# Performance work log

Measured on AMD Instinct MI355X. Metric: run time of the kernel, lower is better.

The kernel has to match this reference:

```python
import jax, jax.numpy as jnp
import numpy as np

HEADS = 16
DIM_HEAD = 128
SCALE = DIM_HEAD ** -0.5


def rotate_half(x):
    # x: (..., d) with d even; pairs (x1, x2) -> (-x2, x1)
    x = x.reshape(*x.shape[:-1], -1, 2)
    x1, x2 = x[..., 0], x[..., 1]
    return jnp.stack([-x2, x1], axis=-1).reshape(*x.shape[:-2], -1)


def apply_rotary(freqs, t):
    # freqs: (n, d), t: (b, h, n, d)
    cos = jnp.cos(freqs)[None, None]
    sin = jnp.sin(freqs)[None, None]
    return t * cos + rotate_half(t) * sin


def setup_inputs() -> dict:
    key = jax.random.key(0)
    ks = jax.random.split(key, 6)
    b, n, dim = 2, 2048, 2048
    inner = HEADS * DIM_HEAD
    s = dim ** -0.5
    x = jax.random.normal(ks[0], (b, n, dim), dtype=jnp.float32)
    rotary_emb = jax.random.normal(ks[1], (n, DIM_HEAD), dtype=jnp.float32)
    Wq = jax.random.normal(ks[2], (dim, inner), dtype=jnp.float32) * s
    Wkv = jax.random.normal(ks[3], (dim, 2 * inner), dtype=jnp.float32) * s
    Wo = jax.random.normal(ks[4], (inner, dim), dtype=jnp.float32) * s
    bo = jnp.zeros((dim,), dtype=jnp.float32)
    return {"x": x, "rotary_emb": rotary_emb, "Wq": Wq, "Wkv": Wkv, "Wo": Wo, "bo": bo}


def reference(x, rotary_emb, Wq, Wkv, Wo, bo):
    b, n, _ = x.shape
    q = x @ Wq                      # (b, n, inner)
    kv = x @ Wkv                    # (b, n, 2*inner)
    k, v = jnp.split(kv, 2, axis=-1)
    # b n (h d) -> b h n d
    split = lambda t: t.reshape(b, n, HEADS, DIM_HEAD).transpose(0, 2, 1, 3)
    q, k, v = split(q), split(k), split(v)
    q = apply_rotary(rotary_emb, q)
    k = apply_rotary(rotary_emb, k)
    q = q * SCALE
    dots = jnp.einsum('bhid,bhjd->bhij', q, k)
    attn = jax.nn.softmax(dots, axis=-1)
    out = jnp.einsum('bhij,bhjd->bhid', attn, v)
    out = out.transpose(0, 2, 1, 3).reshape(b, n, HEADS * DIM_HEAD)
    return out @ Wo + bo
```

## Files before the change

### kernel.cpp

```cpp
#include <hip/hip_runtime.h>
#include <stdint.h>

typedef __attribute__((ext_vector_type(8))) short s16x8;
typedef __attribute__((ext_vector_type(4))) float f32x4;

#define DEVFN static __device__ __forceinline__

constexpr int   S_LEN = 2048;
constexpr int   DH    = 128;
constexpr int   INNER = 2048;
constexpr float ASCALE = 0.08838834764831845f;

DEVFN float b2f(unsigned short u) {
  union { unsigned int i; float f; } v; v.i = ((unsigned int)u) << 16; return v.f;
}
DEVFN unsigned short f2b(float f) {
  union { float f; unsigned int i; } v; v.f = f;
  unsigned int r = v.i + 0x7fffu + ((v.i >> 16) & 1u);
  return (unsigned short)(r >> 16);
}
DEVFN void async_cp16(const unsigned short* g, unsigned short* l) {
  __builtin_amdgcn_global_load_lds((const __attribute__((address_space(1))) void*)g,
                                   (__attribute__((address_space(3))) void*)l, 16, 0, 0);
}

__global__ __launch_bounds__(256) void cvt_bf16_k(const float* __restrict__ in,
                                                  unsigned short* __restrict__ out) {
  const size_t e = ((size_t)blockIdx.x * 256 + threadIdx.x) * 8;
  const float4 a = *(const float4*)(in + e);
  const float4 b = *(const float4*)(in + e + 4);
  union { s16x8 v; unsigned short u[8]; } o;
  o.u[0] = f2b(a.x); o.u[1] = f2b(a.y); o.u[2] = f2b(a.z); o.u[3] = f2b(a.w);
  o.u[4] = f2b(b.x); o.u[5] = f2b(b.y); o.u[6] = f2b(b.z); o.u[7] = f2b(b.w);
  *(s16x8*)(out + e) = o.v;
}

__global__ __launch_bounds__(256) void rot_cs_k(const float* __restrict__ rot,
                                                float2* __restrict__ cst) {
  const int idx = blockIdx.x * 256 + threadIdx.x;
  const float f = rot[idx];
  float s, c;
  __sincosf(f, &s, &c);
  cst[idx] = make_float2(c, s);
}

__global__ __launch_bounds__(256) void transpose_cvt_k(const float* __restrict__ in,
                                                       unsigned short* __restrict__ out,
                                                       int R, int C) {
  __shared__ __align__(16) unsigned short tile[64][72];
  const int t  = threadIdx.x;
  const int lr = t >> 3;
  const int lc = (t & 7) << 3;
  const size_t ibase = (size_t)blockIdx.y * 64 * C + (size_t)blockIdx.x * 64;
#pragma unroll
  for (int rr = 0; rr < 64; rr += 32) {
    const float* p = in + ibase + (size_t)(rr + lr) * C + lc;
    const float4 a = *(const float4*)p;
    const float4 b = *(const float4*)(p + 4);
    unsigned short* tp = &tile[rr + lr][lc];
    tp[0] = f2b(a.x); tp[1] = f2b(a.y); tp[2] = f2b(a.z); tp[3] = f2b(a.w);
    tp[4] = f2b(b.x); tp[5] = f2b(b.y); tp[6] = f2b(b.z); tp[7] = f2b(b.w);
  }
  __syncthreads();
  const size_t obase = (size_t)blockIdx.x * 64 * R + (size_t)blockIdx.y * 64;
#pragma unroll
  for (int rr = 0; rr < 64; rr += 32) {
    int oc = rr + lr;
    union { s16x8 v; unsigned short s[8]; } u;
#pragma unroll
    for (int j = 0; j < 8; ++j) u.s[j] = tile[lc + j][oc];
    *(s16x8*)(out + obase + (size_t)oc * R + lc) = u.v;
  }
}

__global__ __launch_bounds__(512, 2) void gemm256_qkv(
    const unsigned short* __restrict__ A,
    const unsigned short* __restrict__ Bt,
    unsigned short* __restrict__ out0,
    unsigned short* __restrict__ out1,
    unsigned short* __restrict__ out2,
    const float2* __restrict__ rotcs) {
  constexpr int K = 2048, NT = 32;
  __shared__ __align__(16) unsigned short smem[65536];
  const int tid = threadIdx.x;
  const int wid = tid >> 6, lane = tid & 63;
  const int wm = wid >> 2, wn = wid & 3;
  const int quad = lane >> 4, l15 = lane & 15, l7 = l15 & 7;

  const int lin = blockIdx.x;
  const int logical = (lin & 7) * 48 + (lin >> 3);
  const int m0 = (logical & 15) * 256;
  const int n0 = (logical >> 4) * 256;

  const int r0 = tid >> 3, c0 = tid & 7;

  f32x4 acc[8][4];
#pragma unroll
  for (int i = 0; i < 8; ++i)
#pragma unroll
    for (int j = 0; j < 4; ++j) acc[i][j] = {0.f, 0.f, 0.f, 0.f};

  auto stageA = [&](int t, int h) {
#pragma unroll
    for (int s = 0; s < 2; ++s) {
      const int r = s * 64 + r0;
      async_cp16(A + (size_t)(m0 + h * 128 + r) * K + t * 64 + ((c0 ^ (r0 & 7)) << 3),
                 smem + ((t & 1) * 2 + h) * 8192 + s * 4096 + tid * 8);
    }
  };
  auto stageB = [&](int t, int h) {
#pragma unroll
    for (int s = 0; s < 2; ++s) {
      const int r = s * 64 + r0;
      async_cp16(Bt + (size_t)(n0 + h * 128 + r) * K + t * 64 + ((c0 ^ (r0 & 7)) << 3),
                 smem + 32768 + ((t & 1) * 2 + h) * 8192 + s * 4096 + tid * 8);
    }
  };

  stageA(0, 0); stageA(0, 1); stageB(0, 0); stageB(0, 1);
  stageB(1, 0); stageB(1, 1);
  asm volatile("s_waitcnt vmcnt(4)" ::: "memory");
  __builtin_amdgcn_s_barrier();

#pragma unroll 2
  for (int t = 0; t < NT; ++t) {
    const int cur = t & 1;
    const unsigned short* Ab = smem + (cur * 2 + wm) * 8192;
    const unsigned short* Bb = smem + 32768 + (cur * 2 + (wn >> 1)) * 8192;
    const int bln = (wn & 1) * 64;
    s16x8 bf[4][2];
#pragma unroll
    for (int p = 0; p < 4; ++p) {
      s16x8 af[2][2];
#pragma unroll
      for (int j = 0; j < 2; ++j)
#pragma unroll
        for (int kk = 0; kk < 2; ++kk)
          af[j][kk] = *(const s16x8*)(Ab + ((2 * p + j) * 16 + l15) * 64 + (((kk * 4 + quad) ^ l7) << 3));
      if (p == 0) {
#pragma unroll
        for (int nf = 0; nf < 4; ++nf)
#pragma unroll
          for (int kk = 0; kk < 2; ++kk)
            bf[nf][kk] = *(const s16x8*)(Bb + (bln + nf * 16 + l15) * 64 + (((kk * 4 + quad) ^ l7) << 3));
      }
      if (p == 0 && t + 1 < NT) stageA(t + 1, 0);
      if (p == 1 && t + 1 < NT) stageA(t + 1, 1);
      if (p == 2 && t + 2 < NT) stageB(t + 2, 0);
      if (p == 3 && t + 2 < NT) stageB(t + 2, 1);
      __builtin_amdgcn_s_barrier();
      asm volatile("s_waitcnt lgkmcnt(0)" ::: "memory");
      __builtin_amdgcn_sched_barrier(0);
      __builtin_amdgcn_s_setprio(1);
#pragma unroll
      for (int kk = 0; kk < 2; ++kk)
#pragma unroll
        for (int j = 0; j < 2; ++j)
#pragma unroll
          for (int nf = 0; nf < 4; ++nf)
            acc[2 * p + j][nf] = __builtin_amdgcn_mfma_f32_16x16x32_bf16(af[j][kk], bf[nf][kk], acc[2 * p + j][nf], 0, 0, 0);
      __builtin_amdgcn_s_setprio(0);
      __builtin_amdgcn_sched_barrier(0);
      if (p == 3) {
        if (t == NT - 2)      asm volatile("s_waitcnt vmcnt(0)" ::: "memory");
        else if (t < NT - 2)  asm volatile("s_waitcnt vmcnt(4)" ::: "memory");
      }
      __builtin_amdgcn_s_barrier();
    }
  }

  __syncthreads();
  const int b = m0 >> 11, ibase = m0 & 2047;
  if (n0 < 2 * INNER) {
    const bool isq = (n0 < INNER);
    const int hbase = (n0 & (INNER - 1)) >> 7;
#pragma unroll
    for (int mf = 0; mf < 8; ++mf)
#pragma unroll
      for (int nf = 0; nf < 4; ++nf) {
        const int jl = wn * 64 + nf * 16 + l15;
        const int dd = jl & 127;
        const int cl = jl >> 3;
#pragma unroll
        for (int r = 0; r < 4; ++r) {
          const int il = wm * 128 + mf * 16 + quad * 4 + r;
          const float v  = acc[mf][nf][r];
          const float vp = __shfl_xor(v, 1);
          const float2 cs = rotcs[(size_t)(ibase + il) * 128 + dd];
          float rv = (dd & 1) ? fmaf(v, cs.x,  vp * cs.y)
                              : fmaf(v, cs.x, -vp * cs.y);
          if (isq) rv *= ASCALE;
          smem[il * 256 + ((cl ^ (il & 7)) << 3) + (jl & 7)] = f2b(rv);
        }
      }
    __syncthreads();
    unsigned short* outp = (isq ? out0 : out1) +
                           ((size_t)((b << 4) + hbase) * S_LEN + ibase) * DH;
#pragma unroll
    for (int it = 0; it < 16; ++it) {
      const int f  = it * 512 + tid;
      const int il = f >> 5, cl = f & 31;
      s16x8 vv = *(const s16x8*)(smem + il * 256 + ((cl ^ (il & 7)) << 3));
      const int hh = cl >> 4, dd0 = (cl & 15) << 3;
      *(s16x8*)(outp + (size_t)hh * S_LEN * DH + (size_t)il * DH + dd0) = vv;
    }
  } else {
    const int hbase = (n0 - 2 * INNER) >> 7;
#pragma unroll
    for (int mf = 0; mf < 8; ++mf)
#pragma unroll
      for (int nf = 0; nf < 4; ++nf) {
        const int jl = wn * 64 + nf * 16 + l15;
#pragma unroll
        for (int r = 0; r < 4; ++r) {
          const int il = wm * 128 + mf * 16 + quad * 4 + r;
          const int ci = il >> 3;
          smem[jl * 256 + ((ci ^ (jl & 7)) << 3) + (il & 7)] = f2b(acc[mf][nf][r]);
        }
      }
    __syncthreads();
    unsigned short* outp = out2 + (size_t)((b << 4) + hbase) * DH * S_LEN + ibase;
#pragma unroll
    for (int it = 0; it < 16; ++it) {
      const int f  = it * 512 + tid;
      const int jl = f >> 5, ci = f & 31;
      s16x8 vv = *(const s16x8*)(smem + jl * 256 + ((ci ^ (jl & 7)) << 3));
      const int hh = jl >> 7, dd = jl & 127;
      *(s16x8*)(outp + (size_t)hh * DH * S_LEN + (size_t)dd * S_LEN + (ci << 3)) = vv;
    }
  }
}

template <int EPI>
__global__ __launch_bounds__(256) void gemm_bt(
    const unsigned short* __restrict__ A,
    const unsigned short* __restrict__ Bt,
    float* __restrict__ outf,
    const float* __restrict__ biasf,
    int M, int N, int K) {
  __shared__ __align__(16) unsigned short smem[16384];
  unsigned short* As = smem;
  unsigned short* Bs = smem + 8192;
  const int tid  = threadIdx.x;
  const int wave = tid >> 6, lane = tid & 63;
  const int wm = wave & 1, wn = wave >> 1;
  const int quad = lane >> 4, l15 = lane & 15;
  const int l7 = l15 & 7;
  const int m0 = blockIdx.x * 128, n0 = blockIdx.y * 128;

  f32x4 acc[4][4];
#pragma unroll
  for (int i = 0; i < 4; ++i)
#pragma unroll
    for (int j = 0; j < 4; ++j) acc[i][j] = {0.f, 0.f, 0.f, 0.f};

  const int lrow = lane >> 3;
  const int lchk = (lane & 7) ^ (lrow & 7);
  const unsigned short* a_g = A  + (size_t)(m0 + wave * 32 + lrow) * K + (lchk << 3);
  const unsigned short* b_g = Bt + (size_t)(n0 + wave * 32 + lrow) * K + (lchk << 3);
  unsigned short* As_w = As + (wave * 32) * 64;
  unsigned short* Bs_w = Bs + (wave * 32) * 64;

  for (int k0 = 0; k0 < K; k0 += 64) {
    __syncthreads();
#pragma unroll
    for (int t = 0; t < 4; ++t) {
      async_cp16(a_g + k0 + (size_t)(t * 8) * K, As_w + t * 8 * 64);
      async_cp16(b_g + k0 + (size_t)(t * 8) * K, Bs_w + t * 8 * 64);
    }
    __syncthreads();
#pragma unroll
    for (int ks = 0; ks < 2; ++ks) {
      s16x8 af[4], bfr[4];
#pragma unroll
      for (int mi = 0; mi < 4; ++mi)
        af[mi] = *(const s16x8*)(As + (wm * 64 + mi * 16 + l15) * 64 + (((ks * 4 + quad) ^ l7) << 3));
#pragma unroll
      for (int ni = 0; ni < 4; ++ni)
        bfr[ni] = *(const s16x8*)(Bs + (wn * 64 + ni * 16 + l15) * 64 + (((ks * 4 + quad) ^ l7) << 3));
#pragma unroll
      for (int mi = 0; mi < 4; ++mi)
#pragma unroll
        for (int ni = 0; ni < 4; ++ni)
          acc[mi][ni] = __builtin_amdgcn_mfma_f32_16x16x32_bf16(af[mi], bfr[ni], acc[mi][ni], 0, 0, 0);
    }
  }

#pragma unroll
  for (int mi = 0; mi < 4; ++mi)
#pragma unroll
    for (int ni = 0; ni < 4; ++ni)
#pragma unroll
      for (int r = 0; r < 4; ++r) {
        const int gm = m0 + wm * 64 + mi * 16 + quad * 4 + r;
        const int gn = n0 + wn * 64 + ni * 16 + l15;
        outf[(size_t)gm * N + gn] = acc[mi][ni][r] + biasf[gn];
      }
}

DEVFN void stage_tile(const unsigned short* kh, const unsigned short* vh,
                      int j0, unsigned short* KsB, unsigned short* VsB, int tid) {
#pragma unroll
  for (int v = 0; v < 4; ++v) {
    const int off = v * 2048 + tid * 8;
    const int kr = off >> 7;
    const int kc = (((off & 127) >> 3) ^ (kr & 7)) << 3;
    async_cp16(kh + (size_t)(j0 + kr) * DH + kc, KsB + off);
    const int vr = off >> 6;
    const int vc = (((off & 63) >> 3) ^ (vr & 7)) << 3;
    async_cp16(vh + (size_t)vr * S_LEN + j0 + vc, VsB + off);
  }
}

__global__ __launch_bounds__(256, 2) void flash_attn(
    const unsigned short* __restrict__ q,
    const unsigned short* __restrict__ k,
    const unsigned short* __restrict__ vt,
    unsigned short* __restrict__ aout) {
  __shared__ __align__(16) unsigned short Ks[2][64 * 128];
  __shared__ __align__(16) unsigned short Vs[2][128 * 64];
  __shared__ __align__(16) unsigned short Ps[4][32 * 64];
  const int tid = threadIdx.x;
  const int w = tid >> 6, lane = tid & 63;
  const int quad = lane >> 4, l15 = lane & 15;
  const int l7 = l15 & 7;

  const int lin  = blockIdx.y * 16 + blockIdx.x;
  const int xcd  = lin & 7, slot = lin >> 3;
  const int bh   = (xcd << 2) + (slot >> 4);
  const int i0   = (slot & 15) * 128;

  const unsigned short* qh = q  + (size_t)bh * S_LEN * DH;
  const unsigned short* kh = k  + (size_t)bh * S_LEN * DH;
  const unsigned short* vh = vt + (size_t)bh * DH * S_LEN;

  s16x8 qf[2][4];
#pragma unroll
  for (int mi = 0; mi < 2; ++mi)
#pragma unroll
    for (int ks = 0; ks < 4; ++ks)
      qf[mi][ks] = *(const s16x8*)(qh + (size_t)(i0 + w * 32 + mi * 16 + l15) * DH + ks * 32 + quad * 8);

  f32x4 oacc[2][8];
#pragma unroll
  for (int mi = 0; mi < 2; ++mi)
#pragma unroll
    for (int ni = 0; ni < 8; ++ni) oacc[mi][ni] = {0.f, 0.f, 0.f, 0.f};
  float mrun[2][4], lrun[2][4];
#pragma unroll
  for (int mi = 0; mi < 2; ++mi)
#pragma unroll
    for (int r = 0; r < 4; ++r) { mrun[mi][r] = -1e30f; lrun[mi][r] = 0.f; }

  unsigned short* Pw = Ps[w];

  stage_tile(kh, vh, 0, Ks[0], Vs[0], tid);
  __syncthreads();
  int cur = 0;

  for (int j0 = 0; j0 < S_LEN; j0 += 64) {
    if (j0 + 64 < S_LEN)
      stage_tile(kh, vh, j0 + 64, Ks[cur ^ 1], Vs[cur ^ 1], tid);
    const unsigned short* Ksc = Ks[cur];
    const unsigned short* Vsc = Vs[cur];

    f32x4 sacc[2][4];
#pragma unroll
    for (int mi = 0; mi < 2; ++mi)
#pragma unroll
      for (int ni = 0; ni < 4; ++ni) sacc[mi][ni] = {0.f, 0.f, 0.f, 0.f};
#pragma unroll
    for (int ks = 0; ks < 4; ++ks) {
      s16x8 kb[4];
#pragma unroll
      for (int ni = 0; ni < 4; ++ni)
        kb[ni] = *(const s16x8*)(Ksc + (ni * 16 + l15) * 128 + (((ks * 4 + quad) ^ l7) << 3));
#pragma unroll
      for (int mi = 0; mi < 2; ++mi)
#pragma unroll
        for (int ni = 0; ni < 4; ++ni)
          sacc[mi][ni] = __builtin_amdgcn_mfma_f32_16x16x32_bf16(qf[mi][ks], kb[ni], sacc[mi][ni], 0, 0, 0);
    }

    float al[2][4];
    int anyresc = 0;
#pragma unroll
    for (int mi = 0; mi < 2; ++mi)
#pragma unroll
      for (int r = 0; r < 4; ++r) {
        float v = fmaxf(fmaxf(sacc[mi][0][r], sacc[mi][1][r]),
                        fmaxf(sacc[mi][2][r], sacc[mi][3][r]));
        v = fmaxf(v, __shfl_xor(v, 1));
        v = fmaxf(v, __shfl_xor(v, 2));
        v = fmaxf(v, __shfl_xor(v, 4));
        v = fmaxf(v, __shfl_xor(v, 8));
        const float mo   = mrun[mi][r];
        const int   resc = v > mo + 8.f;
        const float mnew = resc ? v : mo;
        const float a    = resc ? __expf(mo - v) : 1.f;
        mrun[mi][r] = mnew;
        al[mi][r]   = a;
        anyresc |= resc;
        float s0 = 0.f;
#pragma unroll
        for (int ni = 0; ni < 4; ++ni) {
          float p = __expf(sacc[mi][ni][r] - mnew);
          sacc[mi][ni][r] = p;
          s0 += p;
        }
        lrun[mi][r] = lrun[mi][r] * a + s0;
      }
    if (__any(anyresc)) {
#pragma unroll
      for (int mi = 0; mi < 2; ++mi)
#pragma unroll
        for (int ni = 0; ni < 8; ++ni)
#pragma unroll
          for (int r = 0; r < 4; ++r) oacc[mi][ni][r] *= al[mi][r];
    }

#pragma unroll
    for (int mi = 0; mi < 2; ++mi)
#pragma unroll
      for (int ni = 0; ni < 4; ++ni) {
        const int col = ni * 16 + l15;
        const int ch  = col >> 3;
#pragma unroll
        for (int r = 0; r < 4; ++r) {
          const int row = mi * 16 + quad * 4 + r;
          Pw[row * 64 + ((ch ^ (row & 7)) << 3) + (col & 7)] = f2b(sacc[mi][ni][r]);
        }
      }
    __threadfence_block();

#pragma unroll
    for (int ks = 0; ks < 2; ++ks) {
      const int swz = ((ks * 4 + quad) ^ l7) << 3;
      s16x8 pf[2];
#pragma unroll
      for (int mi = 0; mi < 2; ++mi)
        pf[mi] = *(const s16x8*)(Pw + (mi * 16 + l15) * 64 + swz);
#pragma unroll
      for (int ni = 0; ni < 8; ++ni) {
        s16x8 vb = *(const s16x8*)(Vsc + (ni * 16 + l15) * 64 + swz);
#pragma unroll
        for (int mi = 0; mi < 2; ++mi)
          oacc[mi][ni] = __builtin_amdgcn_mfma_f32_16x16x32_bf16(pf[mi], vb, oacc[mi][ni], 0, 0, 0);
      }
    }

    __syncthreads();
    cur ^= 1;
  }

  const int b = bh >> 4, h = bh & 15;
#pragma unroll
  for (int mi = 0; mi < 2; ++mi)
#pragma unroll
    for (int r = 0; r < 4; ++r) {
      float l = lrun[mi][r];
      l += __shfl_xor(l, 1);
      l += __shfl_xor(l, 2);
      l += __shfl_xor(l, 4);
      l += __shfl_xor(l, 8);
      const float inv = 1.0f / l;
      const int i = i0 + w * 32 + mi * 16 + quad * 4 + r;
#pragma unroll
      for (int ni = 0; ni < 8; ++ni) {
        const int dd = ni * 16 + l15;
        aout[((size_t)b * S_LEN + i) * INNER + h * DH + dd] = f2b(oacc[mi][ni][r] * inv);
      }
    }
}

extern "C" void kernel_launch(void* const* d_in, const int* in_sizes, int n_in,
                              void* d_out, int out_size, void* d_ws, size_t ws_size,
                              hipStream_t stream) {
  const float* x   = (const float*)d_in[0];
  const float* rot = (const float*)d_in[1];
  const float* Wq  = (const float*)d_in[2];
  const float* Wkv = (const float*)d_in[3];
  const float* Wo  = (const float*)d_in[4];
  const float* bo  = (const float*)d_in[5];
  float* out = (float*)d_out;

  unsigned short* ws = (unsigned short*)d_ws;
  unsigned short* wt  = ws;
  unsigned short* wot = wt  + (size_t)6144 * 2048;
  unsigned short* qb  = wot + (size_t)2048 * 2048;
  unsigned short* kb  = qb  + (size_t)32 * 2048 * 128;
  unsigned short* vtb = kb  + (size_t)32 * 2048 * 128;
  unsigned short* xb  = vtb + (size_t)32 * 2048 * 128;
  unsigned short* att = wt;

  float2* cst = (float2*)d_out;

  rot_cs_k<<<dim3(1024), 256, 0, stream>>>(rot, cst);
  cvt_bf16_k<<<dim3(4096), 256, 0, stream>>>(x, xb);
  transpose_cvt_k<<<dim3(32, 32), 256, 0, stream>>>(Wq,  wt, 2048, 2048);
  transpose_cvt_k<<<dim3(64, 32), 256, 0, stream>>>(Wkv, wt + (size_t)2048 * 2048, 2048, 4096);
  transpose_cvt_k<<<dim3(32, 32), 256, 0, stream>>>(Wo,  wot, 2048, 2048);

  gemm256_qkv<<<dim3(384), 512, 0, stream>>>(xb, wt, qb, kb, vtb, cst);
  flash_attn<<<dim3(16, 32), 256, 0, stream>>>(qb, kb, vtb, att);
  gemm_bt<1><<<dim3(32, 16), 256, 0, stream>>>(att, wot, out, bo, 4096, 2048, 2048);
}
```

Before: 432.4 us.

## Split fused QKV GEMM into QK GEMM and separate V GEMM kernel

The fused 256x256-tile QKV projection launches 384 blocks. It is split into a QK-only launch of 256 blocks with the rotary epilogue, plus a V projection through the 128x128 gemm_bt kernel, which gains a transposed bf16 epilogue. The goal is to remove the partial second wave of the large-tile kernel on a 256-CU device. In exchange it adds a kernel launch and runs the V projection on a smaller-tile GEMM, which may be less efficient.

New measurement: 412.1 us. 4.7% less time.

```diff
diff --git a/kernel.cpp b/kernel.cpp
--- a/kernel.cpp
+++ b/kernel.cpp
@@ -73,12 +73,11 @@
   }
 }
 
-__global__ __launch_bounds__(512, 2) void gemm256_qkv(
+__global__ __launch_bounds__(512, 2) void gemm256_qk(
     const unsigned short* __restrict__ A,
     const unsigned short* __restrict__ Bt,
     unsigned short* __restrict__ out0,
     unsigned short* __restrict__ out1,
-    unsigned short* __restrict__ out2,
     const float2* __restrict__ rotcs) {
   constexpr int K = 2048, NT = 32;
   __shared__ __align__(16) unsigned short smem[65536];
@@ -88,7 +87,7 @@
   const int quad = lane >> 4, l15 = lane & 15, l7 = l15 & 7;
 
   const int lin = blockIdx.x;
-  const int logical = (lin & 7) * 48 + (lin >> 3);
+  const int logical = (lin & 7) * 32 + (lin >> 3);
   const int m0 = (logical & 15) * 256;
   const int n0 = (logical >> 4) * 256;
 
@@ -171,63 +170,37 @@
 
   __syncthreads();
   const int b = m0 >> 11, ibase = m0 & 2047;
-  if (n0 < 2 * INNER) {
-    const bool isq = (n0 < INNER);
-    const int hbase = (n0 & (INNER - 1)) >> 7;
-#pragma unroll
-    for (int mf = 0; mf < 8; ++mf)
-#pragma unroll
-      for (int nf = 0; nf < 4; ++nf) {
-        const int jl = wn * 64 + nf * 16 + l15;
-        const int dd = jl & 127;
-        const int cl = jl >> 3;
-#pragma unroll
-        for (int r = 0; r < 4; ++r) {
-          const int il = wm * 128 + mf * 16 + quad * 4 + r;
-          const float v  = acc[mf][nf][r];
-          const float vp = __shfl_xor(v, 1);
-          const float2 cs = rotcs[(size_t)(ibase + il) * 128 + dd];
-          float rv = (dd & 1) ? fmaf(v, cs.x,  vp * cs.y)
-                              : fmaf(v, cs.x, -vp * cs.y);
-          if (isq) rv *= ASCALE;
-          smem[il * 256 + ((cl ^ (il & 7)) << 3) + (jl & 7)] = f2b(rv);
-        }
-      }
-    __syncthreads();
-    unsigned short* outp = (isq ? out0 : out1) +
-                           ((size_t)((b << 4) + hbase) * S_LEN + ibase) * DH;
-#pragma unroll
-    for (int it = 0; it < 16; ++it) {
-      const int f  = it * 512 + tid;
-      const int il = f >> 5, cl = f & 31;
-      s16x8 vv = *(const s16x8*)(smem + il * 256 + ((cl ^ (il & 7)) << 3));
-      const int hh = cl >> 4, dd0 = (cl & 15) << 3;
-      *(s16x8*)(outp + (size_t)hh * S_LEN * DH + (size_t)il * DH + dd0) = vv;
-    }
-  } else {
-    const int hbase = (n0 - 2 * INNER) >> 7;
-#pragma unroll
-    for (int mf = 0; mf < 8; ++mf)
-#pragma unroll
-      for (int nf = 0; nf < 4; ++nf) {
-        const int jl = wn * 64 + nf * 16 + l15;
-#pragma unroll
-        for (int r = 0; r < 4; ++r) {
-          const int il = wm * 128 + mf * 16 + quad * 4 + r;
-          const int ci = il >> 3;
-          smem[jl * 256 + ((ci ^ (jl & 7)) << 3) + (il & 7)] = f2b(acc[mf][nf][r]);
-        }
-      }
-    __syncthreads();
-    unsigned short* outp = out2 + (size_t)((b << 4) + hbase) * DH * S_LEN + ibase;
-#pragma unroll
-    for (int it = 0; it < 16; ++it) {
-      const int f  = it * 512 + tid;
-      const int jl = f >> 5, ci = f & 31;
-      s16x8 vv = *(const s16x8*)(smem + jl * 256 + ((ci ^ (jl & 7)) << 3));
-      const int hh = jl >> 7, dd = jl & 127;
-      *(s16x8*)(outp + (size_t)hh * DH * S_LEN + (size_t)dd * S_LEN + (ci << 3)) = vv;
-    }
+  const bool isq = (n0 < INNER);
+  const int hbase = (n0 & (INNER - 1)) >> 7;
+#pragma unroll
+  for (int mf = 0; mf < 8; ++mf)
+#pragma unroll
+    for (int nf = 0; nf < 4; ++nf) {
+      const int jl = wn * 64 + nf * 16 + l15;
+      const int dd = jl & 127;
+      const int cl = jl >> 3;
+#pragma unroll
+      for (int r = 0; r < 4; ++r) {
+        const int il = wm * 128 + mf * 16 + quad * 4 + r;
+        const float v  = acc[mf][nf][r];
+        const float vp = __shfl_xor(v, 1);
+        const float2 cs = rotcs[(size_t)(ibase + il) * 128 + dd];
+        float rv = (dd & 1) ? fmaf(v, cs.x,  vp * cs.y)
+                            : fmaf(v, cs.x, -vp * cs.y);
+        if (isq) rv *= ASCALE;
+        smem[il * 256 + ((cl ^ (il & 7)) << 3) + (jl & 7)] = f2b(rv);
+      }
+    }
+  __syncthreads();
+  unsigned short* outp = (isq ? out0 : out1) +
+                         ((size_t)((b << 4) + hbase) * S_LEN + ibase) * DH;
+#pragma unroll
+  for (int it = 0; it < 16; ++it) {
+    const int f  = it * 512 + tid;
+    const int il = f >> 5, cl = f & 31;
+    s16x8 vv = *(const s16x8*)(smem + il * 256 + ((cl ^ (il & 7)) << 3));
+    const int hh = cl >> 4, dd0 = (cl & 15) << 3;
+    *(s16x8*)(outp + (size_t)hh * S_LEN * DH + (size_t)il * DH + dd0) = vv;
   }
 }
 
@@ -235,6 +208,7 @@
 __global__ __launch_bounds__(256) void gemm_bt(
     const unsigned short* __restrict__ A,
     const unsigned short* __restrict__ Bt,
+    unsigned short* __restrict__ out2,
     float* __restrict__ outf,
     const float* __restrict__ biasf,
     int M, int N, int K) {
@@ -286,16 +260,42 @@
     }
   }
 
-#pragma unroll
-  for (int mi = 0; mi < 4; ++mi)
-#pragma unroll
-    for (int ni = 0; ni < 4; ++ni)
-#pragma unroll
-      for (int r = 0; r < 4; ++r) {
-        const int gm = m0 + wm * 64 + mi * 16 + quad * 4 + r;
-        const int gn = n0 + wn * 64 + ni * 16 + l15;
-        outf[(size_t)gm * N + gn] = acc[mi][ni][r] + biasf[gn];
-      }
+  if constexpr (EPI == 1) {
+#pragma unroll
+    for (int mi = 0; mi < 4; ++mi)
+#pragma unroll
+      for (int ni = 0; ni < 4; ++ni)
+#pragma unroll
+        for (int r = 0; r < 4; ++r) {
+          const int gm = m0 + wm * 64 + mi * 16 + quad * 4 + r;
+          const int gn = n0 + wn * 64 + ni * 16 + l15;
+          outf[(size_t)gm * N + gn] = acc[mi][ni][r] + biasf[gn];
+        }
+  } else {
+    __syncthreads();
+    const int b = m0 >> 11, ibase = m0 & 2047;
+    const int h = n0 >> 7;
+#pragma unroll
+    for (int mi = 0; mi < 4; ++mi)
+#pragma unroll
+      for (int ni = 0; ni < 4; ++ni) {
+        const int dd = wn * 64 + ni * 16 + l15;
+#pragma unroll
+        for (int r = 0; r < 4; ++r) {
+          const int il = wm * 64 + mi * 16 + quad * 4 + r;
+          smem[dd * 128 + (((il >> 3) ^ (dd & 7)) << 3) + (il & 7)] = f2b(acc[mi][ni][r]);
+        }
+      }
+    __syncthreads();
+    unsigned short* outp = out2 + (size_t)((b << 4) + h) * DH * S_LEN + ibase;
+#pragma unroll
+    for (int it = 0; it < 8; ++it) {
+      const int f  = it * 256 + tid;
+      const int dd = f >> 4, ch = f & 15;
+      s16x8 vv = *(const s16x8*)(smem + dd * 128 + ((ch ^ (dd & 7)) << 3));
+      *(s16x8*)(outp + (size_t)dd * S_LEN + (ch << 3)) = vv;
+    }
+  }
 }
 
 DEVFN void stage_tile(const unsigned short* kh, const unsigned short* vh,
@@ -501,7 +501,9 @@
   transpose_cvt_k<<<dim3(64, 32), 256, 0, stream>>>(Wkv, wt + (size_t)2048 * 2048, 2048, 4096);
   transpose_cvt_k<<<dim3(32, 32), 256, 0, stream>>>(Wo,  wot, 2048, 2048);
 
-  gemm256_qkv<<<dim3(384), 512, 0, stream>>>(xb, wt, qb, kb, vtb, cst);
+  gemm256_qk<<<dim3(256), 512, 0, stream>>>(xb, wt, qb, kb, cst);
+  gemm_bt<2><<<dim3(32, 16), 256, 0, stream>>>(xb, wt + (size_t)4096 * 2048, vtb,
+                                               nullptr, nullptr, 4096, 2048, 2048);
   flash_attn<<<dim3(16, 32), 256, 0, stream>>>(qb, kb, vtb, att);
-  gemm_bt<1><<<dim3(32, 16), 256, 0, stream>>>(att, wot, out, bo, 4096, 2048, 2048);
-}
+  gemm_bt<1><<<dim3(32, 16), 256, 0, stream>>>(att, wot, nullptr, out, bo, 4096, 2048, 2048);
+}
```
